# Kernel tuning notes

Hardware: AMD Instinct MI355X
Metric: run time of the kernel (lower is better)

## Reference

```python
import jax, jax.numpy as jnp
import numpy as np

GROUPS = 32
EPS = 1e-5
N_HEADS = 8


def setup_inputs() -> dict:
    key = jax.random.key(0)
    ks = jax.random.split(key, 12)
    B, H, W, C = 16, 64, 64, 512
    Nctx, Dctx = 77, 768
    s_c = 1.0 / np.sqrt(C)
    s_ctx = 1.0 / np.sqrt(Dctx)
    return {
        "x": jax.random.normal(ks[0], (B, H, W, C), jnp.float32),
        "context": jax.random.normal(ks[1], (B, Nctx, Dctx), jnp.float32),
        "gn_scale": jnp.ones((C,), jnp.float32),
        "gn_bias": jnp.zeros((C,), jnp.float32),
        "wq": jax.random.normal(ks[2], (C, C), jnp.float32) * s_c,
        "bq": jnp.zeros((C,), jnp.float32),
        "wk": jax.random.normal(ks[3], (Dctx, C), jnp.float32) * s_ctx,
        "bk": jnp.zeros((C,), jnp.float32),
        "wv": jax.random.normal(ks[4], (Dctx, C), jnp.float32) * s_ctx,
        "bv": jnp.zeros((C,), jnp.float32),
        "wo": jax.random.normal(ks[5], (C, C), jnp.float32) * s_c,
        "bo": jnp.zeros((C,), jnp.float32),
    }


def _group_norm(x, scale, bias):
    B, H, W, C = x.shape
    xg = x.reshape(B, H, W, GROUPS, C // GROUPS)
    mean = jnp.mean(xg, axis=(1, 2, 4), keepdims=True)
    var = jnp.var(xg, axis=(1, 2, 4), keepdims=True)
    xn = (xg - mean) * jax.lax.rsqrt(var + EPS)
    return xn.reshape(B, H, W, C) * scale + bias


def reference(x, context, gn_scale, gn_bias, wq, bq, wk, bk, wv, bv, wo, bo):
    B, H, W, C = x.shape
    head_dim = C // N_HEADS
    h = _group_norm(x, gn_scale, gn_bias)
    h_flat = h.reshape(B, H * W, C)
    Q = h_flat @ wq + bq                      # [B, N, C]
    K = context @ wk + bk                     # [B, Nctx, C]
    V = context @ wv + bv

    def split_heads(t):
        b, n, c = t.shape
        return t.reshape(b, n, N_HEADS, head_dim).transpose(0, 2, 1, 3)

    Qh, Kh, Vh = split_heads(Q), split_heads(K), split_heads(V)
    scale = 1.0 / jnp.sqrt(jnp.asarray(head_dim, x.dtype))
    scores = jnp.einsum('bhid,bhjd->bhij', Qh, Kh) * scale
    attn = jax.nn.softmax(scores, axis=-1)
    out = jnp.einsum('bhij,bhjd->bhid', attn, Vh)  # [B, h, N, d]
    out = out.transpose(0, 2, 1, 3).reshape(B, H * W, C)
    out = out @ wo + bo
    return out.reshape(B, H, W, C) + x
```

## Files before the change

kernel.cpp:

```cpp
#include <hip/hip_runtime.h>
#include <hip/hip_bf16.h>

typedef __attribute__((ext_vector_type(4))) float f32x4;
typedef __attribute__((ext_vector_type(8))) short bf16x8;
typedef unsigned short u16;

#define AS1 __attribute__((address_space(1)))
#define AS3 __attribute__((address_space(3)))

#define B_    16
#define HW_   4096
#define C_    512
#define NCTX  77
#define DCTX  768
#define NH    8
#define HD    64
#define EPSV  1e-5f

__device__ inline u16 f2bf(float f) {
    union { float f; unsigned u; } v; v.f = f;
    unsigned r = v.u + 0x7fffu + ((v.u >> 16) & 1u);
    return (u16)(r >> 16);
}

__global__ __launch_bounds__(256) void gn_trans(const float* __restrict__ x,
                                                float* __restrict__ mean,
                                                float* __restrict__ rstd,
                                                const float* __restrict__ wq,
                                                const float* __restrict__ wk,
                                                const float* __restrict__ wv,
                                                const float* __restrict__ wo,
                                                u16* __restrict__ wqT,
                                                u16* __restrict__ wkT,
                                                u16* __restrict__ wvT,
                                                u16* __restrict__ woT) {
    if (blockIdx.x < 512) {
        int b = blockIdx.x >> 5, g = blockIdx.x & 31;
        const float* px = x + (size_t)b * HW_ * C_ + g * 16;
        float s = 0.f, ss = 0.f;
        for (int t = threadIdx.x; t < HW_ * 4; t += 256) {
            int hw = t >> 2, c4 = (t & 3) * 4;
            const float4 v = *(const float4*)(px + (size_t)hw * C_ + c4);
            s  += v.x + v.y + v.z + v.w;
            ss += v.x * v.x + v.y * v.y + v.z * v.z + v.w * v.w;
        }
        for (int off = 32; off; off >>= 1) { s += __shfl_xor(s, off); ss += __shfl_xor(ss, off); }
        __shared__ float red[2][4];
        int wv_ = threadIdx.x >> 6, lane = threadIdx.x & 63;
        if (lane == 0) { red[0][wv_] = s; red[1][wv_] = ss; }
        __syncthreads();
        if (threadIdx.x == 0) {
            float S = red[0][0] + red[0][1] + red[0][2] + red[0][3];
            float SS = red[1][0] + red[1][1] + red[1][2] + red[1][3];
            float mn = S / 65536.f;
            float var = SS / 65536.f - mn * mn;
            mean[blockIdx.x] = mn;
            rstd[blockIdx.x] = rsqrtf(var + EPSV);
        }
    } else {
        int idx = (blockIdx.x - 512) * 256 + threadIdx.x;
        if (idx < 262144) {
            int k = idx >> 9, n = idx & 511;
            wqT[(size_t)n * 512 + k] = f2bf(wq[idx]);
        } else if (idx < 655360) {
            int i = idx - 262144;
            int k = i >> 9, n = i & 511;
            wkT[(size_t)n * 768 + k] = f2bf(wk[i]);
        } else if (idx < 1048576) {
            int i = idx - 655360;
            int k = i >> 9, n = i & 511;
            wvT[(size_t)n * 768 + k] = f2bf(wv[i]);
        } else if (idx < 1310720) {
            int i = idx - 1048576;
            int k = i >> 9, n = i & 511;
            woT[(size_t)n * 512 + k] = f2bf(wo[i]);
        }
    }
}

__global__ __launch_bounds__(256) void gemm_kv(const float* __restrict__ A,
                                               const u16* __restrict__ wkT,
                                               const u16* __restrict__ wvT,
                                               const float* __restrict__ bk,
                                               const float* __restrict__ bv,
                                               u16* __restrict__ kb,
                                               u16* __restrict__ vb) {
    constexpr int M = 1232, K = 768;
    __shared__ __align__(16) u16 As[128][40];
    __shared__ __align__(16) u16 Bs[128][40];
    int bx = blockIdx.x;
    const u16* Bt = (bx < 4) ? wkT : wvT;
    const float* bias = (bx < 4) ? bk : bv;
    u16* out = (bx < 4) ? kb : vb;
    int tid = threadIdx.x, lane = tid & 63, wid = tid >> 6;
    int wm = wid >> 1, wn = wid & 1;
    int row0 = blockIdx.y * 128, col0 = (bx & 3) * 128;
    int q = lane >> 4, r16 = lane & 15;

    f32x4 acc[4][4];
#pragma unroll
    for (int i = 0; i < 4; i++)
#pragma unroll
        for (int j = 0; j < 4; j++) acc[i][j] = (f32x4){0.f, 0.f, 0.f, 0.f};

    for (int k0 = 0; k0 < K; k0 += 32) {
#pragma unroll
        for (int it = 0; it < 2; ++it) {
            int e = it * 256 + tid;
            int rr = e >> 2, kc = (e & 3) * 8;
            int ga = row0 + rr; if (ga > M - 1) ga = M - 1;
            float4 a0 = *(const float4*)(A + (size_t)ga * K + k0 + kc);
            float4 a1 = *(const float4*)(A + (size_t)ga * K + k0 + kc + 4);
            bf16x8 av;
            av[0] = (short)f2bf(a0.x); av[1] = (short)f2bf(a0.y);
            av[2] = (short)f2bf(a0.z); av[3] = (short)f2bf(a0.w);
            av[4] = (short)f2bf(a1.x); av[5] = (short)f2bf(a1.y);
            av[6] = (short)f2bf(a1.z); av[7] = (short)f2bf(a1.w);
            *(bf16x8*)&As[rr][kc] = av;
            int gb = col0 + rr;
            bf16x8 bv8 = *(const bf16x8*)(Bt + (size_t)gb * K + k0 + kc);
            *(bf16x8*)&Bs[rr][kc] = bv8;
        }
        __syncthreads();
        bf16x8 afr[4], bfr[4];
#pragma unroll
        for (int mi = 0; mi < 4; mi++) afr[mi] = *(const bf16x8*)&As[wm * 64 + mi * 16 + r16][q * 8];
#pragma unroll
        for (int ni = 0; ni < 4; ni++) bfr[ni] = *(const bf16x8*)&Bs[wn * 64 + ni * 16 + r16][q * 8];
#pragma unroll
        for (int mi = 0; mi < 4; mi++)
#pragma unroll
            for (int ni = 0; ni < 4; ni++)
                acc[mi][ni] = __builtin_amdgcn_mfma_f32_16x16x32_bf16(afr[mi], bfr[ni], acc[mi][ni], 0, 0, 0);
        __syncthreads();
    }

#pragma unroll
    for (int mi = 0; mi < 4; mi++) {
#pragma unroll
        for (int rr = 0; rr < 4; rr++) {
            int grow = row0 + wm * 64 + mi * 16 + q * 4 + rr;
            if (grow >= M) continue;
#pragma unroll
            for (int ni = 0; ni < 4; ni++) {
                int gcol = col0 + wn * 64 + ni * 16 + r16;
                float v = acc[mi][ni][rr] + bias[gcol];
                out[(size_t)grow * 512 + gcol] = f2bf(v);
            }
        }
    }
}

__global__ __launch_bounds__(256, 2) void gemm_fusedq(const float* __restrict__ x,
                                                      const float* __restrict__ mean,
                                                      const float* __restrict__ rstd,
                                                      const float* __restrict__ gns,
                                                      const float* __restrict__ gnb,
                                                      const u16* __restrict__ Bt,
                                                      const float* __restrict__ bias,
                                                      u16* __restrict__ out) {
    constexpr int K = 512;
    __shared__ __align__(16) u16 LA[2][8192];
    __shared__ __align__(16) u16 LB[2][8192];
    int tid = threadIdx.x, lane = tid & 63, wid = tid >> 6;
    int wr = wid >> 1, wc = wid & 1;
    int q = lane >> 4, r16 = lane & 15;

    int orig = blockIdx.x;
    int wg = (orig & 7) * 256 + (orig >> 3);
    int bx = wg & 3, by = wg >> 2;
    int row0 = by * 128, col0 = bx * 128;

    int srow = tid >> 3;
    int schunk = (tid & 7) ^ (srow & 7);
    const u16* gB = Bt + (size_t)(col0 + srow) * K + schunk * 8;
    const int lo = tid * 8;

    int c8 = tid & 7;
    int rbase = (tid >> 3) * 4;
    const float* xb = x + (size_t)(row0 + rbase) * 512 + c8 * 8;
    int bg0 = (row0 >> 12) * 32;

    f32x4 acc[4][4];
#pragma unroll
    for (int i = 0; i < 4; i++)
#pragma unroll
        for (int j = 0; j < 4; j++) acc[i][j] = (f32x4){0.f, 0.f, 0.f, 0.f};

    float4 ar[8];
    float mn, rs;
    float4 s0v, s1v, b0v, b1v;

#define LOADA(kt) do { _Pragma("unroll")                                          \
    for (int i_ = 0; i_ < 4; ++i_) {                                              \
        ar[2 * i_]     = *(const float4*)(xb + (kt) * 64 + (size_t)i_ * 512);     \
        ar[2 * i_ + 1] = *(const float4*)(xb + (kt) * 64 + (size_t)i_ * 512 + 4); \
    } } while (0)

#define LOADP(kt) do { int c0_ = (kt) * 64 + c8 * 8; int bg_ = bg0 + (c0_ >> 4);  \
    mn = mean[bg_]; rs = rstd[bg_];                                               \
    s0v = *(const float4*)(gns + c0_); s1v = *(const float4*)(gns + c0_ + 4);     \
    b0v = *(const float4*)(gnb + c0_); b1v = *(const float4*)(gnb + c0_ + 4);     \
  } while (0)

#define WRITEA(nbuf) do {                                                         \
    float m2_[8], a2_[8];                                                         \
    m2_[0]=rs*s0v.x; m2_[1]=rs*s0v.y; m2_[2]=rs*s0v.z; m2_[3]=rs*s0v.w;           \
    m2_[4]=rs*s1v.x; m2_[5]=rs*s1v.y; m2_[6]=rs*s1v.z; m2_[7]=rs*s1v.w;           \
    a2_[0]=b0v.x-mn*m2_[0]; a2_[1]=b0v.y-mn*m2_[1];                               \
    a2_[2]=b0v.z-mn*m2_[2]; a2_[3]=b0v.w-mn*m2_[3];                               \
    a2_[4]=b1v.x-mn*m2_[4]; a2_[5]=b1v.y-mn*m2_[5];                               \
    a2_[6]=b1v.z-mn*m2_[6]; a2_[7]=b1v.w-mn*m2_[7];                               \
    _Pragma("unroll")                                                             \
    for (int i_ = 0; i_ < 4; ++i_) {                                              \
        int row_ = rbase + i_;                                                    \
        bf16x8 pk_;                                                               \
        pk_[0]=(short)f2bf(ar[2*i_].x  *m2_[0]+a2_[0]);                           \
        pk_[1]=(short)f2bf(ar[2*i_].y  *m2_[1]+a2_[1]);                           \
        pk_[2]=(short)f2bf(ar[2*i_].z  *m2_[2]+a2_[2]);                           \
        pk_[3]=(short)f2bf(ar[2*i_].w  *m2_[3]+a2_[3]);                           \
        pk_[4]=(short)f2bf(ar[2*i_+1].x*m2_[4]+a2_[4]);                           \
        pk_[5]=(short)f2bf(ar[2*i_+1].y*m2_[5]+a2_[5]);                           \
        pk_[6]=(short)f2bf(ar[2*i_+1].z*m2_[6]+a2_[6]);                           \
        pk_[7]=(short)f2bf(ar[2*i_+1].w*m2_[7]+a2_[7]);                           \
        *(bf16x8*)&LA[nbuf][row_ * 64 + ((c8 ^ (row_ & 7)) * 8)] = pk_;           \
    } } while (0)

#define STG_B(kt, s) __builtin_amdgcn_global_load_lds( \
        (const AS1 void*)(gB + (kt) * 64 + (size_t)((s) * 32) * K), \
        (AS3 void*)(&LB[(kt) & 1][(s) * 2048 + lo]), 16, 0, 0)

#define PHASE_(buf, h, ks) do {                                                            \
    bf16x8 afr[2], bfr[4];                                                                 \
    const int ch_ = (((ks) * 4 + q) ^ (r16 & 7)) * 8;                                      \
    _Pragma("unroll")                                                                      \
    for (int mi = 0; mi < 2; mi++)                                                         \
        afr[mi] = *(const bf16x8*)&LA[buf][(wr * 64 + ((h) * 2 + mi) * 16 + r16) * 64 + ch_]; \
    _Pragma("unroll")                                                                      \
    for (int ni = 0; ni < 4; ni++)                                                         \
        bfr[ni] = *(const bf16x8*)&LB[buf][(wc * 64 + ni * 16 + r16) * 64 + ch_];          \
    __builtin_amdgcn_s_setprio(1);                                                         \
    _Pragma("unroll")                                                                      \
    for (int mi = 0; mi < 2; mi++)                                                         \
      _Pragma("unroll")                                                                    \
      for (int ni = 0; ni < 4; ni++)                                                       \
        acc[(h) * 2 + mi][ni] =                                                            \
            __builtin_amdgcn_mfma_f32_16x16x32_bf16(afr[mi], bfr[ni], acc[(h) * 2 + mi][ni], 0, 0, 0); \
    __builtin_amdgcn_s_setprio(0);                                                         \
  } while (0)

    LOADA(0); LOADP(0);
    asm volatile("" ::: "memory");
    STG_B(0, 0); STG_B(0, 1); STG_B(0, 2); STG_B(0, 3);
    asm volatile("s_waitcnt vmcnt(4)" ::: "memory");
    WRITEA(0);
    asm volatile("s_waitcnt lgkmcnt(0)" ::: "memory");

#pragma unroll
    for (int t = 0; t < 7; ++t) {
        const int buf = t & 1;
        LOADA(t + 1); LOADP(t + 1);
        asm volatile("" ::: "memory");
        STG_B(t + 1, 0); STG_B(t + 1, 1); STG_B(t + 1, 2); STG_B(t + 1, 3);
        asm volatile("s_waitcnt vmcnt(18)" ::: "memory");
        __builtin_amdgcn_s_barrier();
        asm volatile("" ::: "memory");
        PHASE_(buf, 0, 0); PHASE_(buf, 1, 0); PHASE_(buf, 0, 1); PHASE_(buf, 1, 1);
        asm volatile("s_waitcnt vmcnt(4)" ::: "memory");
        WRITEA(buf ^ 1);
        asm volatile("s_waitcnt lgkmcnt(0)" ::: "memory");
        __builtin_amdgcn_s_barrier();
        asm volatile("" ::: "memory");
    }
    asm volatile("s_waitcnt vmcnt(0) lgkmcnt(0)" ::: "memory");
    __builtin_amdgcn_s_barrier();
    asm volatile("" ::: "memory");
    PHASE_(1, 0, 0); PHASE_(1, 1, 0); PHASE_(1, 0, 1); PHASE_(1, 1, 1);
#undef LOADA
#undef LOADP
#undef WRITEA
#undef STG_B
#undef PHASE_

#pragma unroll
    for (int mi = 0; mi < 4; mi++) {
#pragma unroll
        for (int rr = 0; rr < 4; rr++) {
            int grow = row0 + wr * 64 + mi * 16 + q * 4 + rr;
#pragma unroll
            for (int ni = 0; ni < 4; ni++) {
                int gcol = col0 + wc * 64 + ni * 16 + r16;
                float v = acc[mi][ni][rr] + bias[gcol];
                out[(size_t)grow * 512 + gcol] = f2bf(v);
            }
        }
    }
}

__global__ __launch_bounds__(256, 4) void gemm_ring(const u16* __restrict__ A,
                                                    const u16* __restrict__ Bt,
                                                    const float* __restrict__ bias,
                                                    const float* __restrict__ res,
                                                    float* __restrict__ out) {
    constexpr int K = 512;
    __shared__ __align__(16) u16 LA[2][4096];
    __shared__ __align__(16) u16 LB[2][4096];
    int tid = threadIdx.x, lane = tid & 63, wid = tid >> 6;
    int wr = wid >> 1, wc = wid & 1;
    int q = lane >> 4, r16 = lane & 15;

    int orig = blockIdx.x;
    int wg = (orig & 7) * 256 + (orig >> 3);
    int bx = wg & 3, by = wg >> 2;
    int row0 = by * 128, col0 = bx * 128;

    int srow = tid >> 2;
    int schunk = (tid & 3) ^ (srow & 3);
    const u16* gA = A + (size_t)(row0 + srow) * K + schunk * 8;
    const u16* gB = Bt + (size_t)(col0 + srow) * K + schunk * 8;
    const int lo = tid * 8;

    f32x4 acc[4][4];
#pragma unroll
    for (int i = 0; i < 4; i++)
#pragma unroll
        for (int j = 0; j < 4; j++) acc[i][j] = (f32x4){0.f, 0.f, 0.f, 0.f};

#define STG(kt) do { int sl_ = (kt) & 1;                                              \
    __builtin_amdgcn_global_load_lds((const AS1 void*)(gA + (kt) * 32),               \
                                     (AS3 void*)(&LA[sl_][lo]), 16, 0, 0);            \
    __builtin_amdgcn_global_load_lds((const AS1 void*)(gA + (kt) * 32 + (size_t)64 * K), \
                                     (AS3 void*)(&LA[sl_][2048 + lo]), 16, 0, 0);     \
    __builtin_amdgcn_global_load_lds((const AS1 void*)(gB + (kt) * 32),               \
                                     (AS3 void*)(&LB[sl_][lo]), 16, 0, 0);            \
    __builtin_amdgcn_global_load_lds((const AS1 void*)(gB + (kt) * 32 + (size_t)64 * K), \
                                     (AS3 void*)(&LB[sl_][2048 + lo]), 16, 0, 0);     \
  } while (0)

#define COMPUTE(sl) do {                                                              \
    bf16x8 afr[4], bfr[4];                                                            \
    const int ch_ = (q ^ (r16 & 3)) * 8;                                              \
    _Pragma("unroll")                                                                 \
    for (int mi = 0; mi < 4; mi++)                                                    \
        afr[mi] = *(const bf16x8*)&LA[sl][(wr * 64 + mi * 16 + r16) * 32 + ch_];      \
    _Pragma("unroll")                                                                 \
    for (int ni = 0; ni < 4; ni++)                                                    \
        bfr[ni] = *(const bf16x8*)&LB[sl][(wc * 64 + ni * 16 + r16) * 32 + ch_];      \
    __builtin_amdgcn_s_setprio(1);                                                    \
    _Pragma("unroll")                                                                 \
    for (int mi = 0; mi < 4; mi++)                                                    \
      _Pragma("unroll")                                                               \
      for (int ni = 0; ni < 4; ni++)                                                  \
        acc[mi][ni] = __builtin_amdgcn_mfma_f32_16x16x32_bf16(afr[mi], bfr[ni], acc[mi][ni], 0, 0, 0); \
    __builtin_amdgcn_s_setprio(0);                                                    \
  } while (0)

    STG(0);
#pragma unroll
    for (int t = 0; t < 15; ++t) {
        STG(t + 1);
        asm volatile("s_waitcnt vmcnt(4)" ::: "memory");
        asm volatile("s_barrier" ::: "memory");
        COMPUTE(t & 1);
        asm volatile("s_barrier" ::: "memory");
    }
    asm volatile("s_waitcnt vmcnt(0)" ::: "memory");
    asm volatile("s_barrier" ::: "memory");
    COMPUTE(1);
#undef STG
#undef COMPUTE

#pragma unroll
    for (int mi = 0; mi < 4; mi++) {
#pragma unroll
        for (int rr = 0; rr < 4; rr++) {
            int grow = row0 + wr * 64 + mi * 16 + q * 4 + rr;
#pragma unroll
            for (int ni = 0; ni < 4; ni++) {
                int gcol = col0 + wc * 64 + ni * 16 + r16;
                float v = acc[mi][ni][rr] + bias[gcol];
                size_t idx = (size_t)grow * 512 + gcol;
                out[idx] = v + res[idx];
            }
        }
    }
}

__global__ __launch_bounds__(256) void attn_mfma(const u16* __restrict__ Qb,
                                                 const u16* __restrict__ Kb,
                                                 const u16* __restrict__ Vb,
                                                 u16* __restrict__ Ob) {
    __shared__ __align__(16) u16 Ks[80][72];
    __shared__ __align__(16) u16 VT[64][104];
    __shared__ __align__(16) u16 Ps[64][104];
    int tid = threadIdx.x, lane = tid & 63, wv = tid >> 6;
    int q = lane >> 4, r16 = lane & 15;
    int tile0 = blockIdx.x * 4;
    int bh = blockIdx.y;
    int b = bh >> 3, h = bh & 7;

    {
        unsigned* p0 = (unsigned*)&Ks[0][0];
        for (int i = tid; i < 2880; i += 256) p0[i] = 0u;
        unsigned* p1 = (unsigned*)&VT[0][0];
        for (int i = tid; i < 3328; i += 256) p1[i] = 0u;
        unsigned* p2 = (unsigned*)&Ps[0][0];
        for (int i = tid; i < 3328; i += 256) p2[i] = 0u;
    }
    __syncthreads();

    size_t kvbase = ((size_t)b * NCTX) * C_ + h * HD;
    for (int c = tid; c < NCTX * 8; c += 256) {
        int j = c >> 3, d8 = (c & 7) * 8;
        *(bf16x8*)&Ks[j][d8] = *(const bf16x8*)(Kb + kvbase + (size_t)j * C_ + d8);
    }
    for (int t = tid; t < NCTX * 64; t += 256) {
        int j = t >> 6, d = t & 63;
        VT[d][j] = Vb[kvbase + (size_t)j * C_ + d];
    }
    __syncthreads();

    const size_t tstep = (size_t)64 * C_;
    const u16* qp = Qb + ((size_t)b * HW_ + wv * 16 + r16) * C_ + h * HD + q * 8;
    bool v4 = (r16 < NCTX - 64);

    bf16x8 qc0 = *(const bf16x8*)(qp + (size_t)tile0 * tstep);
    bf16x8 qc1 = *(const bf16x8*)(qp + (size_t)tile0 * tstep + 32);

    for (int it = 0; it < 4; ++it) {
        int tile = tile0 + it;
        bf16x8 qn0 = qc0, qn1 = qc1;
        if (it < 3) {
            qn0 = *(const bf16x8*)(qp + (size_t)(tile + 1) * tstep);
            qn1 = *(const bf16x8*)(qp + (size_t)(tile + 1) * tstep + 32);
        }

        f32x4 accs[5];
#pragma unroll
        for (int nt = 0; nt < 5; ++nt) accs[nt] = (f32x4){0.f, 0.f, 0.f, 0.f};
#pragma unroll
        for (int nt = 0; nt < 5; ++nt) {
            bf16x8 kf = *(const bf16x8*)&Ks[nt * 16 + r16][q * 8];
            accs[nt] = __builtin_amdgcn_mfma_f32_16x16x32_bf16(qc0, kf, accs[nt], 0, 0, 0);
        }
#pragma unroll
        for (int nt = 0; nt < 5; ++nt) {
            bf16x8 kf = *(const bf16x8*)&Ks[nt * 16 + r16][32 + q * 8];
            accs[nt] = __builtin_amdgcn_mfma_f32_16x16x32_bf16(qc1, kf, accs[nt], 0, 0, 0);
        }

#pragma unroll
        for (int r = 0; r < 4; ++r) {
            float s[5];
#pragma unroll
            for (int nt = 0; nt < 5; ++nt) s[nt] = accs[nt][r] * 0.125f;
            float m = fmaxf(fmaxf(fmaxf(s[0], s[1]), fmaxf(s[2], s[3])), v4 ? s[4] : -3.0e38f);
#pragma unroll
            for (int off = 1; off < 16; off <<= 1) m = fmaxf(m, __shfl_xor(m, off));
            float e[5], sum = 0.f;
#pragma unroll
            for (int nt = 0; nt < 5; ++nt) {
                e[nt] = (nt < 4 || v4) ? __expf(s[nt] - m) : 0.f;
                sum += e[nt];
            }
#pragma unroll
            for (int off = 1; off < 16; off <<= 1) sum += __shfl_xor(sum, off);
            float inv = 1.0f / sum;
            int prow = wv * 16 + q * 4 + r;
#pragma unroll
            for (int nt = 0; nt < 5; ++nt)
                Ps[prow][nt * 16 + r16] = f2bf(e[nt] * inv);
        }

        f32x4 acco[4];
#pragma unroll
        for (int nt = 0; nt < 4; ++nt) acco[nt] = (f32x4){0.f, 0.f, 0.f, 0.f};
#pragma unroll
        for (int ks = 0; ks < 3; ++ks) {
            bf16x8 pf = *(const bf16x8*)&Ps[wv * 16 + r16][ks * 32 + q * 8];
#pragma unroll
            for (int nt = 0; nt < 4; ++nt) {
                bf16x8 vf = *(const bf16x8*)&VT[nt * 16 + r16][ks * 32 + q * 8];
                acco[nt] = __builtin_amdgcn_mfma_f32_16x16x32_bf16(pf, vf, acco[nt], 0, 0, 0);
            }
        }

        int row0 = tile * 64 + wv * 16;
#pragma unroll
        for (int nt = 0; nt < 4; ++nt)
#pragma unroll
            for (int r = 0; r < 4; ++r) {
                int row = row0 + q * 4 + r;
                int col = h * HD + nt * 16 + r16;
                Ob[((size_t)b * HW_ + row) * C_ + col] = f2bf(acco[nt][r]);
            }
        qc0 = qn0; qc1 = qn1;
    }
}

extern "C" void kernel_launch(void* const* d_in, const int* in_sizes, int n_in,
                              void* d_out, int out_size, void* d_ws, size_t ws_size,
                              hipStream_t stream) {
    const float* x   = (const float*)d_in[0];
    const float* ctx = (const float*)d_in[1];
    const float* gns = (const float*)d_in[2];
    const float* gnb = (const float*)d_in[3];
    const float* wq  = (const float*)d_in[4];
    const float* bq  = (const float*)d_in[5];
    const float* wk  = (const float*)d_in[6];
    const float* bk  = (const float*)d_in[7];
    const float* wv  = (const float*)d_in[8];
    const float* bv  = (const float*)d_in[9];
    const float* wo  = (const float*)d_in[10];
    const float* bo  = (const float*)d_in[11];

    char* ws = (char*)d_ws;
    float* mean = (float*)(ws + 0);
    float* rstd = (float*)(ws + 2048);
    u16* wqT  = (u16*)(ws + 4096);
    u16* wkT  = (u16*)(ws + 528384);
    u16* wvT  = (u16*)(ws + 1314816);
    u16* woT  = (u16*)(ws + 2101248);
    u16* aob  = (u16*)(ws + 4517888);
    u16* qb   = (u16*)(ws + 71626752);
    u16* kb   = (u16*)(ws + 138735616);
    u16* vb   = (u16*)(ws + 139997184);

    gn_trans<<<5632, 256, 0, stream>>>(x, mean, rstd, wq, wk, wv, wo, wqT, wkT, wvT, woT);
    gemm_kv<<<dim3(8, 10), 256, 0, stream>>>(ctx, wkT, wvT, bk, bv, kb, vb);

    gemm_fusedq<<<2048, 256, 0, stream>>>(x, mean, rstd, gns, gnb, wqT, bq, qb);

    attn_mfma<<<dim3(16, 128), 256, 0, stream>>>(qb, kb, vb, aob);

    gemm_ring<<<2048, 256, 0, stream>>>(aob, woT, bo, x, (float*)d_out);
}
```

Measured before the change: 293.4 us.

## Use 256x256 triple-buffered output GEMM and double attention tiles per block

The output projection GEMM moves from 128x128 tiles with 256 threads and double buffering to 256x256 tiles with 512 threads and three LDS buffers. A and B loads are split across two half-phases so the next stages stream in while MFMAs run. This cuts global reloads of A and B per output element, but it uses more LDS and registers and allows one block per CU. The attention kernel also processes 8 query tiles per block instead of 4, halving how often K and V are reloaded into shared memory.

Measured after the change: 295.5 us. No clear change (+0.7%).

```diff
diff --git a/kernel.cpp b/kernel.cpp
--- a/kernel.cpp
+++ b/kernel.cpp
@@ -297,84 +297,130 @@
     }
 }
 
-__global__ __launch_bounds__(256, 4) void gemm_ring(const u16* __restrict__ A,
+__global__ __launch_bounds__(512, 1) void gemm_o256(const u16* __restrict__ A,
                                                     const u16* __restrict__ Bt,
                                                     const float* __restrict__ bias,
                                                     const float* __restrict__ res,
                                                     float* __restrict__ out) {
     constexpr int K = 512;
-    __shared__ __align__(16) u16 LA[2][4096];
-    __shared__ __align__(16) u16 LB[2][4096];
+    __shared__ __align__(16) u16 LA[3][8192];
+    __shared__ __align__(16) u16 LB[3][8192];
     int tid = threadIdx.x, lane = tid & 63, wid = tid >> 6;
-    int wr = wid >> 1, wc = wid & 1;
+    int wr = wid >> 2, wc = wid & 3;
     int q = lane >> 4, r16 = lane & 15;
 
     int orig = blockIdx.x;
-    int wg = (orig & 7) * 256 + (orig >> 3);
-    int bx = wg & 3, by = wg >> 2;
-    int row0 = by * 128, col0 = bx * 128;
+    int wg = (orig & 7) * 64 + (orig >> 3);
+    int bx = wg & 1, by = wg >> 1;
+    int row0 = by * 256, col0 = bx * 256;
 
     int srow = tid >> 2;
     int schunk = (tid & 3) ^ (srow & 3);
     const u16* gA = A + (size_t)(row0 + srow) * K + schunk * 8;
     const u16* gB = Bt + (size_t)(col0 + srow) * K + schunk * 8;
-    const int lo = tid * 8;
-
-    f32x4 acc[4][4];
-#pragma unroll
-    for (int i = 0; i < 4; i++)
+
+    f32x4 acc[8][4];
+#pragma unroll
+    for (int i = 0; i < 8; i++)
 #pragma unroll
         for (int j = 0; j < 4; j++) acc[i][j] = (f32x4){0.f, 0.f, 0.f, 0.f};
 
-#define STG(kt) do { int sl_ = (kt) & 1;                                              \
-    __builtin_amdgcn_global_load_lds((const AS1 void*)(gA + (kt) * 32),               \
-                                     (AS3 void*)(&LA[sl_][lo]), 16, 0, 0);            \
-    __builtin_amdgcn_global_load_lds((const AS1 void*)(gA + (kt) * 32 + (size_t)64 * K), \
-                                     (AS3 void*)(&LA[sl_][2048 + lo]), 16, 0, 0);     \
-    __builtin_amdgcn_global_load_lds((const AS1 void*)(gB + (kt) * 32),               \
-                                     (AS3 void*)(&LB[sl_][lo]), 16, 0, 0);            \
-    __builtin_amdgcn_global_load_lds((const AS1 void*)(gB + (kt) * 32 + (size_t)64 * K), \
-                                     (AS3 void*)(&LB[sl_][2048 + lo]), 16, 0, 0);     \
+#define STG_A(kt) do { int b_ = (kt) % 3;                                                \
+    __builtin_amdgcn_global_load_lds((const AS1 void*)(gA + (kt) * 32),                  \
+                                     (AS3 void*)(&LA[b_][tid * 8]), 16, 0, 0);           \
+    __builtin_amdgcn_global_load_lds((const AS1 void*)(gA + (kt) * 32 + (size_t)128 * K),\
+                                     (AS3 void*)(&LA[b_][4096 + tid * 8]), 16, 0, 0);    \
   } while (0)
-
-#define COMPUTE(sl) do {                                                              \
-    bf16x8 afr[4], bfr[4];                                                            \
-    const int ch_ = (q ^ (r16 & 3)) * 8;                                              \
-    _Pragma("unroll")                                                                 \
-    for (int mi = 0; mi < 4; mi++)                                                    \
-        afr[mi] = *(const bf16x8*)&LA[sl][(wr * 64 + mi * 16 + r16) * 32 + ch_];      \
-    _Pragma("unroll")                                                                 \
-    for (int ni = 0; ni < 4; ni++)                                                    \
-        bfr[ni] = *(const bf16x8*)&LB[sl][(wc * 64 + ni * 16 + r16) * 32 + ch_];      \
-    __builtin_amdgcn_s_setprio(1);                                                    \
-    _Pragma("unroll")                                                                 \
-    for (int mi = 0; mi < 4; mi++)                                                    \
-      _Pragma("unroll")                                                               \
-      for (int ni = 0; ni < 4; ni++)                                                  \
-        acc[mi][ni] = __builtin_amdgcn_mfma_f32_16x16x32_bf16(afr[mi], bfr[ni], acc[mi][ni], 0, 0, 0); \
-    __builtin_amdgcn_s_setprio(0);                                                    \
+#define STG_B(kt) do { int b_ = (kt) % 3;                                                \
+    __builtin_amdgcn_global_load_lds((const AS1 void*)(gB + (kt) * 32),                  \
+                                     (AS3 void*)(&LB[b_][tid * 8]), 16, 0, 0);           \
+    __builtin_amdgcn_global_load_lds((const AS1 void*)(gB + (kt) * 32 + (size_t)128 * K),\
+                                     (AS3 void*)(&LB[b_][4096 + tid * 8]), 16, 0, 0);    \
   } while (0)
 
-    STG(0);
-#pragma unroll
-    for (int t = 0; t < 15; ++t) {
-        STG(t + 1);
-        asm volatile("s_waitcnt vmcnt(4)" ::: "memory");
-        asm volatile("s_barrier" ::: "memory");
-        COMPUTE(t & 1);
-        asm volatile("s_barrier" ::: "memory");
-    }
-    asm volatile("s_waitcnt vmcnt(0)" ::: "memory");
-    asm volatile("s_barrier" ::: "memory");
-    COMPUTE(1);
-#undef STG
-#undef COMPUTE
-
-#pragma unroll
-    for (int mi = 0; mi < 4; mi++) {
+#define PHASE_(buf, h) do {                                                              \
+    bf16x8 afr[4], bfr[4];                                                               \
+    const int ch_ = (q ^ (r16 & 3)) * 8;                                                 \
+    _Pragma("unroll")                                                                    \
+    for (int mi = 0; mi < 4; mi++)                                                       \
+        afr[mi] = *(const bf16x8*)&LA[buf][(wr * 128 + (h) * 64 + mi * 16 + r16) * 32 + ch_]; \
+    _Pragma("unroll")                                                                    \
+    for (int ni = 0; ni < 4; ni++)                                                       \
+        bfr[ni] = *(const bf16x8*)&LB[buf][(wc * 64 + ni * 16 + r16) * 32 + ch_];        \
+    __builtin_amdgcn_s_setprio(1);                                                       \
+    _Pragma("unroll")                                                                    \
+    for (int mi = 0; mi < 4; mi++)                                                       \
+      _Pragma("unroll")                                                                  \
+      for (int ni = 0; ni < 4; ni++)                                                     \
+        acc[(h) * 4 + mi][ni] =                                                          \
+            __builtin_amdgcn_mfma_f32_16x16x32_bf16(afr[mi], bfr[ni], acc[(h) * 4 + mi][ni], 0, 0, 0); \
+    __builtin_amdgcn_s_setprio(0);                                                       \
+  } while (0)
+
+    STG_A(0); STG_B(0); STG_A(1); STG_B(1);
+    asm volatile("s_waitcnt vmcnt(4)" ::: "memory");
+    __builtin_amdgcn_s_barrier();
+    asm volatile("" ::: "memory");
+
+#pragma unroll
+    for (int t = 0; t < 16; ++t) {
+        const int buf = t % 3;
+        {
+            bf16x8 afr[4], bfr[4];
+            const int ch_ = (q ^ (r16 & 3)) * 8;
+#pragma unroll
+            for (int mi = 0; mi < 4; mi++)
+                afr[mi] = *(const bf16x8*)&LA[buf][(wr * 128 + mi * 16 + r16) * 32 + ch_];
+#pragma unroll
+            for (int ni = 0; ni < 4; ni++)
+                bfr[ni] = *(const bf16x8*)&LB[buf][(wc * 64 + ni * 16 + r16) * 32 + ch_];
+            if (t < 14) STG_A(t + 2);
+            __builtin_amdgcn_s_barrier();
+            asm volatile("s_waitcnt lgkmcnt(0)" ::: "memory");
+            __builtin_amdgcn_s_setprio(1);
+#pragma unroll
+            for (int mi = 0; mi < 4; mi++)
+#pragma unroll
+                for (int ni = 0; ni < 4; ni++)
+                    acc[mi][ni] = __builtin_amdgcn_mfma_f32_16x16x32_bf16(afr[mi], bfr[ni], acc[mi][ni], 0, 0, 0);
+            __builtin_amdgcn_s_setprio(0);
+            __builtin_amdgcn_s_barrier();
+            asm volatile("" ::: "memory");
+        }
+        {
+            bf16x8 afr[4], bfr[4];
+            const int ch_ = (q ^ (r16 & 3)) * 8;
+#pragma unroll
+            for (int mi = 0; mi < 4; mi++)
+                afr[mi] = *(const bf16x8*)&LA[buf][(wr * 128 + 64 + mi * 16 + r16) * 32 + ch_];
+#pragma unroll
+            for (int ni = 0; ni < 4; ni++)
+                bfr[ni] = *(const bf16x8*)&LB[buf][(wc * 64 + ni * 16 + r16) * 32 + ch_];
+            if (t < 14) STG_B(t + 2);
+            __builtin_amdgcn_s_barrier();
+            asm volatile("s_waitcnt lgkmcnt(0)" ::: "memory");
+            __builtin_amdgcn_s_setprio(1);
+#pragma unroll
+            for (int mi = 0; mi < 4; mi++)
+#pragma unroll
+                for (int ni = 0; ni < 4; ni++)
+                    acc[4 + mi][ni] = __builtin_amdgcn_mfma_f32_16x16x32_bf16(afr[mi], bfr[ni], acc[4 + mi][ni], 0, 0, 0);
+            __builtin_amdgcn_s_setprio(0);
+        }
+        if (t < 14)       asm volatile("s_waitcnt vmcnt(4)" ::: "memory");
+        else if (t == 14) asm volatile("s_waitcnt vmcnt(0)" ::: "memory");
+        __builtin_amdgcn_s_barrier();
+        asm volatile("" ::: "memory");
+    }
+#undef STG_A
+#undef STG_B
+#undef PHASE_
+
+#pragma unroll
+    for (int mi = 0; mi < 8; mi++) {
 #pragma unroll
         for (int rr = 0; rr < 4; rr++) {
-            int grow = row0 + wr * 64 + mi * 16 + q * 4 + rr;
+            int grow = row0 + wr * 128 + mi * 16 + q * 4 + rr;
 #pragma unroll
             for (int ni = 0; ni < 4; ni++) {
                 int gcol = col0 + wc * 64 + ni * 16 + r16;
@@ -395,7 +441,7 @@
     __shared__ __align__(16) u16 Ps[64][104];
     int tid = threadIdx.x, lane = tid & 63, wv = tid >> 6;
     int q = lane >> 4, r16 = lane & 15;
-    int tile0 = blockIdx.x * 4;
+    int tile0 = blockIdx.x * 8;
     int bh = blockIdx.y;
     int b = bh >> 3, h = bh & 7;
 
@@ -427,10 +473,10 @@
     bf16x8 qc0 = *(const bf16x8*)(qp + (size_t)tile0 * tstep);
     bf16x8 qc1 = *(const bf16x8*)(qp + (size_t)tile0 * tstep + 32);
 
-    for (int it = 0; it < 4; ++it) {
+    for (int it = 0; it < 8; ++it) {
         int tile = tile0 + it;
         bf16x8 qn0 = qc0, qn1 = qc1;
-        if (it < 3) {
+        if (it < 7) {
             qn0 = *(const bf16x8*)(qp + (size_t)(tile + 1) * tstep);
             qn1 = *(const bf16x8*)(qp + (size_t)(tile + 1) * tstep + 32);
         }
@@ -531,7 +577,7 @@
 
     gemm_fusedq<<<2048, 256, 0, stream>>>(x, mean, rstd, gns, gnb, wqT, bq, qb);
 
-    attn_mfma<<<dim3(16, 128), 256, 0, stream>>>(qb, kb, vb, aob);
-
-    gemm_ring<<<2048, 256, 0, stream>>>(aob, woT, bo, x, (float*)d_out);
-}
+    attn_mfma<<<dim3(8, 128), 256, 0, stream>>>(qb, kb, vb, aob);
+
+    gemm_o256<<<512, 512, 0, stream>>>(aob, woT, bo, x, (float*)d_out);
+}
```

## Merge K/V projection GEMM into fused Q GEMM launch and double attention tiles per block

Applied to the files above, without the earlier changes.

Folds the separate K/V projection kernel into the fused groupnorm+Q GEMM launch as 80 extra blocks appended after the 2048 Q blocks, sharing a pooled LDS buffer. This removes one kernel launch and lets the small K/V GEMM run alongside the Q GEMM. The attention kernel now processes 8 query tiles per block instead of 4, halving the grid and amortizing the K/V LDS staging. The trade-offs are fewer attention blocks for parallelism and K/V blocks scheduled last, which can add a tail.

Result: faster. 281.6 us, median of 3 (-4.0%).

```diff
diff --git a/kernel.cpp b/kernel.cpp
--- a/kernel.cpp
+++ b/kernel.cpp
@@ -78,79 +78,6 @@
     }
 }
 
-__global__ __launch_bounds__(256) void gemm_kv(const float* __restrict__ A,
-                                               const u16* __restrict__ wkT,
-                                               const u16* __restrict__ wvT,
-                                               const float* __restrict__ bk,
-                                               const float* __restrict__ bv,
-                                               u16* __restrict__ kb,
-                                               u16* __restrict__ vb) {
-    constexpr int M = 1232, K = 768;
-    __shared__ __align__(16) u16 As[128][40];
-    __shared__ __align__(16) u16 Bs[128][40];
-    int bx = blockIdx.x;
-    const u16* Bt = (bx < 4) ? wkT : wvT;
-    const float* bias = (bx < 4) ? bk : bv;
-    u16* out = (bx < 4) ? kb : vb;
-    int tid = threadIdx.x, lane = tid & 63, wid = tid >> 6;
-    int wm = wid >> 1, wn = wid & 1;
-    int row0 = blockIdx.y * 128, col0 = (bx & 3) * 128;
-    int q = lane >> 4, r16 = lane & 15;
-
-    f32x4 acc[4][4];
-#pragma unroll
-    for (int i = 0; i < 4; i++)
-#pragma unroll
-        for (int j = 0; j < 4; j++) acc[i][j] = (f32x4){0.f, 0.f, 0.f, 0.f};
-
-    for (int k0 = 0; k0 < K; k0 += 32) {
-#pragma unroll
-        for (int it = 0; it < 2; ++it) {
-            int e = it * 256 + tid;
-            int rr = e >> 2, kc = (e & 3) * 8;
-            int ga = row0 + rr; if (ga > M - 1) ga = M - 1;
-            float4 a0 = *(const float4*)(A + (size_t)ga * K + k0 + kc);
-            float4 a1 = *(const float4*)(A + (size_t)ga * K + k0 + kc + 4);
-            bf16x8 av;
-            av[0] = (short)f2bf(a0.x); av[1] = (short)f2bf(a0.y);
-            av[2] = (short)f2bf(a0.z); av[3] = (short)f2bf(a0.w);
-            av[4] = (short)f2bf(a1.x); av[5] = (short)f2bf(a1.y);
-            av[6] = (short)f2bf(a1.z); av[7] = (short)f2bf(a1.w);
-            *(bf16x8*)&As[rr][kc] = av;
-            int gb = col0 + rr;
-            bf16x8 bv8 = *(const bf16x8*)(Bt + (size_t)gb * K + k0 + kc);
-            *(bf16x8*)&Bs[rr][kc] = bv8;
-        }
-        __syncthreads();
-        bf16x8 afr[4], bfr[4];
-#pragma unroll
-        for (int mi = 0; mi < 4; mi++) afr[mi] = *(const bf16x8*)&As[wm * 64 + mi * 16 + r16][q * 8];
-#pragma unroll
-        for (int ni = 0; ni < 4; ni++) bfr[ni] = *(const bf16x8*)&Bs[wn * 64 + ni * 16 + r16][q * 8];
-#pragma unroll
-        for (int mi = 0; mi < 4; mi++)
-#pragma unroll
-            for (int ni = 0; ni < 4; ni++)
-                acc[mi][ni] = __builtin_amdgcn_mfma_f32_16x16x32_bf16(afr[mi], bfr[ni], acc[mi][ni], 0, 0, 0);
-        __syncthreads();
-    }
-
-#pragma unroll
-    for (int mi = 0; mi < 4; mi++) {
-#pragma unroll
-        for (int rr = 0; rr < 4; rr++) {
-            int grow = row0 + wm * 64 + mi * 16 + q * 4 + rr;
-            if (grow >= M) continue;
-#pragma unroll
-            for (int ni = 0; ni < 4; ni++) {
-                int gcol = col0 + wn * 64 + ni * 16 + r16;
-                float v = acc[mi][ni][rr] + bias[gcol];
-                out[(size_t)grow * 512 + gcol] = f2bf(v);
-            }
-        }
-    }
-}
-
 __global__ __launch_bounds__(256, 2) void gemm_fusedq(const float* __restrict__ x,
                                                       const float* __restrict__ mean,
                                                       const float* __restrict__ rstd,
@@ -158,13 +85,89 @@
                                                       const float* __restrict__ gnb,
                                                       const u16* __restrict__ Bt,
                                                       const float* __restrict__ bias,
-                                                      u16* __restrict__ out) {
+                                                      u16* __restrict__ out,
+                                                      const float* __restrict__ ctx,
+                                                      const u16* __restrict__ wkT,
+                                                      const u16* __restrict__ wvT,
+                                                      const float* __restrict__ bk,
+                                                      const float* __restrict__ bv,
+                                                      u16* __restrict__ kb,
+                                                      u16* __restrict__ vb) {
+    __shared__ __align__(16) u16 POOL[32768];
+    int tid = threadIdx.x, lane = tid & 63, wid = tid >> 6;
+    int q = lane >> 4, r16 = lane & 15;
+
+    if (blockIdx.x >= 2048) {
+        constexpr int M = 1232, K = 768;
+        u16 (*As)[40] = (u16(*)[40])&POOL[0];
+        u16 (*Bs)[40] = (u16(*)[40])&POOL[5120];
+        int idx = blockIdx.x - 2048;
+        int bx = idx & 7, byk = idx >> 3;
+        const u16* Btl = (bx < 4) ? wkT : wvT;
+        const float* bi = (bx < 4) ? bk : bv;
+        u16* o = (bx < 4) ? kb : vb;
+        int wm = wid >> 1, wn = wid & 1;
+        int row0 = byk * 128, col0 = (bx & 3) * 128;
+
+        f32x4 acc[4][4];
+#pragma unroll
+        for (int i = 0; i < 4; i++)
+#pragma unroll
+            for (int j = 0; j < 4; j++) acc[i][j] = (f32x4){0.f, 0.f, 0.f, 0.f};
+
+        for (int k0 = 0; k0 < K; k0 += 32) {
+#pragma unroll
+            for (int it = 0; it < 2; ++it) {
+                int e = it * 256 + tid;
+                int rr = e >> 2, kc = (e & 3) * 8;
+                int ga = row0 + rr; if (ga > M - 1) ga = M - 1;
+                float4 a0 = *(const float4*)(ctx + (size_t)ga * K + k0 + kc);
+                float4 a1 = *(const float4*)(ctx + (size_t)ga * K + k0 + kc + 4);
+                bf16x8 av;
+                av[0] = (short)f2bf(a0.x); av[1] = (short)f2bf(a0.y);
+                av[2] = (short)f2bf(a0.z); av[3] = (short)f2bf(a0.w);
+                av[4] = (short)f2bf(a1.x); av[5] = (short)f2bf(a1.y);
+                av[6] = (short)f2bf(a1.z); av[7] = (short)f2bf(a1.w);
+                *(bf16x8*)&As[rr][kc] = av;
+                int gb = col0 + rr;
+                bf16x8 bv8 = *(const bf16x8*)(Btl + (size_t)gb * K + k0 + kc);
+                *(bf16x8*)&Bs[rr][kc] = bv8;
+            }
+            __syncthreads();
+            bf16x8 afr[4], bfr[4];
+#pragma unroll
+            for (int mi = 0; mi < 4; mi++) afr[mi] = *(const bf16x8*)&As[wm * 64 + mi * 16 + r16][q * 8];
+#pragma unroll
+            for (int ni = 0; ni < 4; ni++) bfr[ni] = *(const bf16x8*)&Bs[wn * 64 + ni * 16 + r16][q * 8];
+#pragma unroll
+            for (int mi = 0; mi < 4; mi++)
+#pragma unroll
+                for (int ni = 0; ni < 4; ni++)
+                    acc[mi][ni] = __builtin_amdgcn_mfma_f32_16x16x32_bf16(afr[mi], bfr[ni], acc[mi][ni], 0, 0, 0);
+            __syncthreads();
+        }
+
+#pragma unroll
+        for (int mi = 0; mi < 4; mi++) {
+#pragma unroll
+            for (int rr = 0; rr < 4; rr++) {
+                int grow = row0 + wm * 64 + mi * 16 + q * 4 + rr;
+                if (grow >= M) continue;
+#pragma unroll
+                for (int ni = 0; ni < 4; ni++) {
+                    int gcol = col0 + wn * 64 + ni * 16 + r16;
+                    float v = acc[mi][ni][rr] + bi[gcol];
+                    o[(size_t)grow * 512 + gcol] = f2bf(v);
+                }
+            }
+        }
+        return;
+    }
+
     constexpr int K = 512;
-    __shared__ __align__(16) u16 LA[2][8192];
-    __shared__ __align__(16) u16 LB[2][8192];
-    int tid = threadIdx.x, lane = tid & 63, wid = tid >> 6;
+    u16 (*LA)[8192] = (u16(*)[8192])&POOL[0];
+    u16 (*LB)[8192] = (u16(*)[8192])&POOL[16384];
     int wr = wid >> 1, wc = wid & 1;
-    int q = lane >> 4, r16 = lane & 15;
 
     int orig = blockIdx.x;
     int wg = (orig & 7) * 256 + (orig >> 3);
@@ -395,7 +398,7 @@
     __shared__ __align__(16) u16 Ps[64][104];
     int tid = threadIdx.x, lane = tid & 63, wv = tid >> 6;
     int q = lane >> 4, r16 = lane & 15;
-    int tile0 = blockIdx.x * 4;
+    int tile0 = blockIdx.x * 8;
     int bh = blockIdx.y;
     int b = bh >> 3, h = bh & 7;
 
@@ -427,10 +430,10 @@
     bf16x8 qc0 = *(const bf16x8*)(qp + (size_t)tile0 * tstep);
     bf16x8 qc1 = *(const bf16x8*)(qp + (size_t)tile0 * tstep + 32);
 
-    for (int it = 0; it < 4; ++it) {
+    for (int it = 0; it < 8; ++it) {
         int tile = tile0 + it;
         bf16x8 qn0 = qc0, qn1 = qc1;
-        if (it < 3) {
+        if (it < 7) {
             qn0 = *(const bf16x8*)(qp + (size_t)(tile + 1) * tstep);
             qn1 = *(const bf16x8*)(qp + (size_t)(tile + 1) * tstep + 32);
         }
@@ -527,11 +530,11 @@
     u16* vb   = (u16*)(ws + 139997184);
 
     gn_trans<<<5632, 256, 0, stream>>>(x, mean, rstd, wq, wk, wv, wo, wqT, wkT, wvT, woT);
-    gemm_kv<<<dim3(8, 10), 256, 0, stream>>>(ctx, wkT, wvT, bk, bv, kb, vb);
-
-    gemm_fusedq<<<2048, 256, 0, stream>>>(x, mean, rstd, gns, gnb, wqT, bq, qb);
-
-    attn_mfma<<<dim3(16, 128), 256, 0, stream>>>(qb, kb, vb, aob);
+
+    gemm_fusedq<<<2128, 256, 0, stream>>>(x, mean, rstd, gns, gnb, wqT, bq, qb,
+                                          ctx, wkT, wvT, bk, bv, kb, vb);
+
+    attn_mfma<<<dim3(8, 128), 256, 0, stream>>>(qb, kb, vb, aob);
 
     gemm_ring<<<2048, 256, 0, stream>>>(aob, woT, bo, x, (float*)d_out);
 }
```
